# Optimization experiments

Hardware: AMD Instinct MI355X
Metric: run time of the kernel (lower is better)

The kernel has to match this reference:

```python
import jax, jax.numpy as jnp
import numpy as np

B, LQ, LK = 8, 1024, 1024
QD, KD, VD, OD, H = 512, 256, 256, 512, 8
HD = OD // H
SCALE = float(np.sqrt(HD))


def setup_inputs() -> dict:
    key = jax.random.key(0)
    ks = jax.random.split(key, 11)
    def lin(k, fan_in, fan_out):
        bound = 1.0 / np.sqrt(fan_in)
        kw, kb = jax.random.split(k)
        W = jax.random.uniform(kw, (fan_in, fan_out), jnp.float32, -bound, bound)
        b = jax.random.uniform(kb, (fan_out,), jnp.float32, -bound, bound)
        return W, b
    Wq, bq = lin(ks[0], QD, OD)
    Wk, bk = lin(ks[1], KD, OD)
    Wv, bv = lin(ks[2], VD, OD)
    Wo, bo = lin(ks[3], OD, OD)
    return {
        "query": jax.random.normal(ks[4], (B, LQ, QD), jnp.float32),
        "key": jax.random.normal(ks[5], (B, LK, KD), jnp.float32),
        "value": jax.random.normal(ks[6], (B, LK, VD), jnp.float32),
        "Wq": Wq, "bq": bq, "Wk": Wk, "bk": bk,
        "Wv": Wv, "bv": bv, "Wo": Wo, "bo": bo,
    }


def reference(query, key, value, Wq, bq, Wk, bk, Wv, bv, Wo, bo):
    b = query.shape[0]
    # project and split heads: (B, H, L, HD)
    q = (query @ Wq + bq).reshape(b, -1, H, HD).transpose(0, 2, 1, 3)
    k = (key @ Wk + bk).reshape(b, -1, H, HD).transpose(0, 2, 1, 3)
    v = (value @ Wv + bv).reshape(b, -1, H, HD).transpose(0, 2, 1, 3)
    scores = jnp.einsum("bhqd,bhkd->bhqk", q, k) / SCALE
    attention = jax.nn.softmax(scores, axis=-1)
    # dropout is identity in eval mode (reference uses eval semantics)
    out = jnp.einsum("bhqk,bhkd->bhqd", attention, v)
    out = out.transpose(0, 2, 1, 3).reshape(b, -1, H * HD)
    out = out @ Wo + bo
    return out, attention
```

## Files before the change

### kernel.cpp

```cpp
#include <hip/hip_runtime.h>

typedef __attribute__((ext_vector_type(8))) short s8b;
typedef __attribute__((ext_vector_type(4))) float f32x4;

#define MFMA_BF16(a, b, c) __builtin_amdgcn_mfma_f32_16x16x32_bf16((a), (b), (c), 0, 0, 0)

__device__ __forceinline__ short f2bf(float f) {
    unsigned u = __float_as_uint(f);
    u += 0x7fffu + ((u >> 16) & 1u);
    return (short)(u >> 16);
}

template <int OMODE, bool ABF16>
__global__ __launch_bounds__(256) void gemm_k(const void* __restrict__ Ain,
                                              const float* __restrict__ W,
                                              const float* __restrict__ bias,
                                              void* __restrict__ Cout,
                                              int K, float scale) {
    __shared__ short As[128][40];
    __shared__ short Bs[128][40];

    const int tid  = threadIdx.x;
    const int lane = tid & 63;
    const int wid  = tid >> 6;
    const int l15  = lane & 15, lhi = lane >> 4;
    const int wr   = wid >> 1, wc = wid & 1;
    const int bm   = blockIdx.x << 7;
    const int bn   = blockIdx.y << 7;

    const f32x4 zf = {0.f, 0.f, 0.f, 0.f};
    f32x4 acc[4][4];
#pragma unroll
    for (int i = 0; i < 4; ++i)
#pragma unroll
        for (int j = 0; j < 4; ++j) acc[i][j] = zf;

    const int arow = tid >> 1;
    const int ak0  = (tid & 1) << 4;
    const int bn_t = tid & 127;
    const int bk0  = (tid >> 7) << 4;

    const int nkt = K >> 5;
    for (int kt = 0; kt < nkt; ++kt) {
        __syncthreads();
        if (ABF16) {
            const short* src = (const short*)Ain + (size_t)(bm + arow) * K + (kt << 5) + ak0;
            *(s8b*)&As[arow][ak0]     = *(const s8b*)(src);
            *(s8b*)&As[arow][ak0 + 8] = *(const s8b*)(src + 8);
        } else {
            const float* src = (const float*)Ain + (size_t)(bm + arow) * K + (kt << 5) + ak0;
            s8b t0, t1;
#pragma unroll
            for (int i = 0; i < 8; ++i) { t0[i] = f2bf(src[i]); t1[i] = f2bf(src[i + 8]); }
            *(s8b*)&As[arow][ak0]     = t0;
            *(s8b*)&As[arow][ak0 + 8] = t1;
        }
        {
            s8b t0, t1;
#pragma unroll
            for (int j = 0; j < 8; ++j)
                t0[j] = f2bf(W[(size_t)((kt << 5) + bk0 + j) * 512 + bn + bn_t]);
#pragma unroll
            for (int j = 0; j < 8; ++j)
                t1[j] = f2bf(W[(size_t)((kt << 5) + bk0 + 8 + j) * 512 + bn + bn_t]);
            *(s8b*)&Bs[bn_t][bk0]     = t0;
            *(s8b*)&Bs[bn_t][bk0 + 8] = t1;
        }
        __syncthreads();
        s8b a[4], b[4];
#pragma unroll
        for (int rt = 0; rt < 4; ++rt)
            a[rt] = *(const s8b*)&As[(wr << 6) + (rt << 4) + l15][lhi << 3];
#pragma unroll
        for (int ct = 0; ct < 4; ++ct)
            b[ct] = *(const s8b*)&Bs[(wc << 6) + (ct << 4) + l15][lhi << 3];
#pragma unroll
        for (int rt = 0; rt < 4; ++rt)
#pragma unroll
            for (int ct = 0; ct < 4; ++ct)
                acc[rt][ct] = MFMA_BF16(a[rt], b[ct], acc[rt][ct]);
    }

#pragma unroll
    for (int rt = 0; rt < 4; ++rt)
#pragma unroll
        for (int ct = 0; ct < 4; ++ct) {
            const int col  = bn + (wc << 6) + (ct << 4) + l15;
            const float bv = bias[col];
#pragma unroll
            for (int r = 0; r < 4; ++r) {
                const int row = bm + (wr << 6) + (rt << 4) + (lhi << 2) + r;
                const float v = (acc[rt][ct][r] + bv) * scale;
                if (OMODE == 0) {
                    ((short*)Cout)[(size_t)row * 512 + col] = f2bf(v);
                } else if (OMODE == 1) {
                    const int bb = row >> 10, kv = row & 1023;
                    ((short*)Cout)[((size_t)(bb * 512 + col) << 10) + kv] = f2bf(v);
                } else {
                    ((float*)Cout)[(size_t)row * 512 + col] = v;
                }
            }
        }
}

__global__ __launch_bounds__(256) void attn_k(const short* __restrict__ Qp,
                                              const short* __restrict__ Kp,
                                              const short* __restrict__ Vt,
                                              float* __restrict__ attn,
                                              short* __restrict__ Oint) {
    __shared__ short Plds[4][32][72];

    const int tid = threadIdx.x;
    const int wid = tid >> 6, lane = tid & 63;
    const int l15 = lane & 15, lhi = lane >> 4;
    const int bid = blockIdx.x;
    const int qc = bid & 7, h = (bid >> 3) & 7, b = bid >> 6;
    const int q0 = (qc << 7) + (wid << 5);

    const size_t qbase = ((size_t)(b * 1024 + q0)) * 512 + h * 64;
    s8b aq[2][2];
#pragma unroll
    for (int rt = 0; rt < 2; ++rt)
#pragma unroll
        for (int ks = 0; ks < 2; ++ks)
            aq[rt][ks] = *(const s8b*)&Qp[qbase + (size_t)((rt << 4) + l15) * 512 + (ks << 5) + (lhi << 3)];

    float m8[8], l8[8];
#pragma unroll
    for (int i = 0; i < 8; ++i) { m8[i] = -1e30f; l8[i] = 0.f; }

    const size_t kbase = ((size_t)(b * 1024)) * 512 + h * 64;

    for (int kt = 0; kt < 16; ++kt) {
        s8b bk[4][2];
#pragma unroll
        for (int c = 0; c < 4; ++c)
#pragma unroll
            for (int ks = 0; ks < 2; ++ks)
                bk[c][ks] = *(const s8b*)&Kp[kbase + (size_t)((kt << 6) + (c << 4) + l15) * 512 + (ks << 5) + (lhi << 3)];
        const f32x4 zf = {0.f, 0.f, 0.f, 0.f};
        f32x4 s[2][4];
#pragma unroll
        for (int rt = 0; rt < 2; ++rt)
#pragma unroll
            for (int c = 0; c < 4; ++c) {
                s[rt][c] = zf;
                s[rt][c] = MFMA_BF16(aq[rt][0], bk[c][0], s[rt][c]);
                s[rt][c] = MFMA_BF16(aq[rt][1], bk[c][1], s[rt][c]);
            }
#pragma unroll
        for (int rt = 0; rt < 2; ++rt)
#pragma unroll
            for (int r = 0; r < 4; ++r) {
                const int idx = (rt << 2) + r;
                const float v0 = s[rt][0][r], v1 = s[rt][1][r];
                const float v2 = s[rt][2][r], v3 = s[rt][3][r];
                const float vm = fmaxf(fmaxf(v0, v1), fmaxf(v2, v3));
                const float mn = fmaxf(m8[idx], vm);
                const float corr = exp2f(m8[idx] - mn);
                const float add = exp2f(v0 - mn) + exp2f(v1 - mn) + exp2f(v2 - mn) + exp2f(v3 - mn);
                l8[idx] = l8[idx] * corr + add;
                m8[idx] = mn;
            }
    }
#pragma unroll
    for (int i = 0; i < 8; ++i) {
        float m = m8[i], l = l8[i];
#pragma unroll
        for (int mask = 1; mask <= 8; mask <<= 1) {
            const float mo = __shfl_xor(m, mask, 64);
            const float lo = __shfl_xor(l, mask, 64);
            const float mn = fmaxf(m, mo);
            l = l * exp2f(m - mn) + lo * exp2f(mo - mn);
            m = mn;
        }
        m8[i] = m;
        l8[i] = 1.0f / l;
    }

    const f32x4 zf = {0.f, 0.f, 0.f, 0.f};
    f32x4 o[2][4];
#pragma unroll
    for (int rt = 0; rt < 2; ++rt)
#pragma unroll
        for (int cd = 0; cd < 4; ++cd) o[rt][cd] = zf;

    const size_t vbase = ((size_t)(((b << 3) + h) << 6)) << 10;
    const size_t abase = ((size_t)(((b << 3) + h) * 1024 + q0)) << 10;

    for (int kt = 0; kt < 16; ++kt) {
        s8b bk[4][2];
#pragma unroll
        for (int c = 0; c < 4; ++c)
#pragma unroll
            for (int ks = 0; ks < 2; ++ks)
                bk[c][ks] = *(const s8b*)&Kp[kbase + (size_t)((kt << 6) + (c << 4) + l15) * 512 + (ks << 5) + (lhi << 3)];
        f32x4 s[2][4];
#pragma unroll
        for (int rt = 0; rt < 2; ++rt)
#pragma unroll
            for (int c = 0; c < 4; ++c) {
                s[rt][c] = zf;
                s[rt][c] = MFMA_BF16(aq[rt][0], bk[c][0], s[rt][c]);
                s[rt][c] = MFMA_BF16(aq[rt][1], bk[c][1], s[rt][c]);
            }
#pragma unroll
        for (int rt = 0; rt < 2; ++rt)
#pragma unroll
            for (int c = 0; c < 4; ++c)
#pragma unroll
                for (int r = 0; r < 4; ++r) {
                    const int idx = (rt << 2) + r;
                    s[rt][c][r] = exp2f(s[rt][c][r] - m8[idx]) * l8[idx];
                }
#pragma unroll
        for (int rt = 0; rt < 2; ++rt)
#pragma unroll
            for (int r = 0; r < 4; ++r) {
                const int prow = (rt << 4) + (lhi << 2) + r;
                const size_t ar = abase + ((size_t)prow << 10) + (kt << 6);
#pragma unroll
                for (int c = 0; c < 4; ++c) {
                    attn[ar + (c << 4) + l15] = s[rt][c][r];
                    Plds[wid][prow][(c << 4) + l15] = f2bf(s[rt][c][r]);
                }
            }
        s8b pa[2][2], bv[4][2];
#pragma unroll
        for (int rt = 0; rt < 2; ++rt)
#pragma unroll
            for (int ks = 0; ks < 2; ++ks)
                pa[rt][ks] = *(const s8b*)&Plds[wid][(rt << 4) + l15][(ks << 5) + (lhi << 3)];
#pragma unroll
        for (int cd = 0; cd < 4; ++cd)
#pragma unroll
            for (int ks = 0; ks < 2; ++ks)
                bv[cd][ks] = *(const s8b*)&Vt[vbase + (size_t)((cd << 4) + l15) * 1024 + (kt << 6) + (ks << 5) + (lhi << 3)];
#pragma unroll
        for (int rt = 0; rt < 2; ++rt)
#pragma unroll
            for (int cd = 0; cd < 4; ++cd) {
                o[rt][cd] = MFMA_BF16(pa[rt][0], bv[cd][0], o[rt][cd]);
                o[rt][cd] = MFMA_BF16(pa[rt][1], bv[cd][1], o[rt][cd]);
            }
    }

#pragma unroll
    for (int rt = 0; rt < 2; ++rt)
#pragma unroll
        for (int cd = 0; cd < 4; ++cd)
#pragma unroll
            for (int r = 0; r < 4; ++r) {
                const size_t orow =
                    ((size_t)(b * 1024 + q0 + (rt << 4) + (lhi << 2) + r)) * 512 + h * 64 + (cd << 4) + l15;
                Oint[orow] = f2bf(o[rt][cd][r]);
            }
}

extern "C" void kernel_launch(void* const* d_in, const int* in_sizes, int n_in,
                              void* d_out, int out_size, void* d_ws, size_t ws_size,
                              hipStream_t stream) {
    (void)in_sizes; (void)n_in; (void)out_size; (void)ws_size;

    const float* query = (const float*)d_in[0];
    const float* key   = (const float*)d_in[1];
    const float* value = (const float*)d_in[2];
    const float* Wq = (const float*)d_in[3];
    const float* bq = (const float*)d_in[4];
    const float* Wk = (const float*)d_in[5];
    const float* bk = (const float*)d_in[6];
    const float* Wv = (const float*)d_in[7];
    const float* bv = (const float*)d_in[8];
    const float* Wo = (const float*)d_in[9];
    const float* bo = (const float*)d_in[10];

    float* out  = (float*)d_out;
    float* attn = out + (size_t)8 * 1024 * 512;

    char* ws    = (char*)d_ws;
    short* Qp   = (short*)(ws);
    short* Kp   = (short*)(ws + (8u << 20));
    short* Vt   = (short*)(ws + (16u << 20));
    short* Oint = (short*)(ws + (24u << 20));

    const dim3 blk(256);
    const dim3 gg(64, 4);
    const float qscale = 0.18033688011112042f;

    gemm_k<0, false><<<gg, blk, 0, stream>>>(query, Wq, bq, Qp, 512, qscale);
    gemm_k<0, false><<<gg, blk, 0, stream>>>(key,   Wk, bk, Kp, 256, 1.0f);
    gemm_k<1, false><<<gg, blk, 0, stream>>>(value, Wv, bv, Vt, 256, 1.0f);
    attn_k<<<dim3(512), blk, 0, stream>>>(Qp, Kp, Vt, attn, Oint);
    gemm_k<2, true><<<gg, blk, 0, stream>>>(Oint, Wo, bo, out, 512, 1.0f);
}
```

Before: 463.1 us.

## Shrink GEMM tiles, add V transpose kernel, vectorize attention stores, remap blocks

The GEMM tile drops from 128x128 to 64x64 and the grid grows, giving more blocks to fill the CUs. The V projection now writes row-major output, and a separate LDS-based kernel transposes it, replacing the scattered strided stores. In the attention kernel, probabilities are staged in fp32 LDS so each wave can write the attention matrix with coalesced 16-byte stores instead of scalar ones. Block indices are also swizzled across batch and head. The cost is less operand reuse per GEMM tile, one extra kernel launch, and a larger workspace.

```diff
diff --git a/kernel.cpp b/kernel.cpp
--- a/kernel.cpp
+++ b/kernel.cpp
@@ -17,90 +17,108 @@
                                               const float* __restrict__ bias,
                                               void* __restrict__ Cout,
                                               int K, float scale) {
-    __shared__ short As[128][40];
-    __shared__ short Bs[128][40];
+    __shared__ short As[64][40];
+    __shared__ short Bs[64][40];
 
     const int tid  = threadIdx.x;
     const int lane = tid & 63;
     const int wid  = tid >> 6;
     const int l15  = lane & 15, lhi = lane >> 4;
     const int wr   = wid >> 1, wc = wid & 1;
-    const int bm   = blockIdx.x << 7;
-    const int bn   = blockIdx.y << 7;
+    const int bm   = blockIdx.x << 6;
+    const int bn   = blockIdx.y << 6;
 
     const f32x4 zf = {0.f, 0.f, 0.f, 0.f};
-    f32x4 acc[4][4];
-#pragma unroll
-    for (int i = 0; i < 4; ++i)
-#pragma unroll
-        for (int j = 0; j < 4; ++j) acc[i][j] = zf;
-
-    const int arow = tid >> 1;
-    const int ak0  = (tid & 1) << 4;
-    const int bn_t = tid & 127;
-    const int bk0  = (tid >> 7) << 4;
+    f32x4 acc[2][2];
+#pragma unroll
+    for (int i = 0; i < 2; ++i)
+#pragma unroll
+        for (int j = 0; j < 2; ++j) acc[i][j] = zf;
+
+    const int arow = tid >> 2;
+    const int ac8  = (tid & 3) << 3;
+    const int bn_t = tid & 63;
+    const int bk0  = (tid >> 6) << 3;
 
     const int nkt = K >> 5;
     for (int kt = 0; kt < nkt; ++kt) {
         __syncthreads();
         if (ABF16) {
-            const short* src = (const short*)Ain + (size_t)(bm + arow) * K + (kt << 5) + ak0;
-            *(s8b*)&As[arow][ak0]     = *(const s8b*)(src);
-            *(s8b*)&As[arow][ak0 + 8] = *(const s8b*)(src + 8);
+            const short* src = (const short*)Ain + (size_t)(bm + arow) * K + (kt << 5) + ac8;
+            *(s8b*)&As[arow][ac8] = *(const s8b*)(src);
         } else {
-            const float* src = (const float*)Ain + (size_t)(bm + arow) * K + (kt << 5) + ak0;
-            s8b t0, t1;
-#pragma unroll
-            for (int i = 0; i < 8; ++i) { t0[i] = f2bf(src[i]); t1[i] = f2bf(src[i + 8]); }
-            *(s8b*)&As[arow][ak0]     = t0;
-            *(s8b*)&As[arow][ak0 + 8] = t1;
+            const float* src = (const float*)Ain + (size_t)(bm + arow) * K + (kt << 5) + ac8;
+            s8b t;
+#pragma unroll
+            for (int i = 0; i < 8; ++i) t[i] = f2bf(src[i]);
+            *(s8b*)&As[arow][ac8] = t;
         }
         {
-            s8b t0, t1;
+            s8b t;
 #pragma unroll
             for (int j = 0; j < 8; ++j)
-                t0[j] = f2bf(W[(size_t)((kt << 5) + bk0 + j) * 512 + bn + bn_t]);
-#pragma unroll
-            for (int j = 0; j < 8; ++j)
-                t1[j] = f2bf(W[(size_t)((kt << 5) + bk0 + 8 + j) * 512 + bn + bn_t]);
-            *(s8b*)&Bs[bn_t][bk0]     = t0;
-            *(s8b*)&Bs[bn_t][bk0 + 8] = t1;
+                t[j] = f2bf(W[(size_t)((kt << 5) + bk0 + j) * 512 + bn + bn_t]);
+            *(s8b*)&Bs[bn_t][bk0] = t;
         }
         __syncthreads();
-        s8b a[4], b[4];
-#pragma unroll
-        for (int rt = 0; rt < 4; ++rt)
-            a[rt] = *(const s8b*)&As[(wr << 6) + (rt << 4) + l15][lhi << 3];
-#pragma unroll
-        for (int ct = 0; ct < 4; ++ct)
-            b[ct] = *(const s8b*)&Bs[(wc << 6) + (ct << 4) + l15][lhi << 3];
-#pragma unroll
-        for (int rt = 0; rt < 4; ++rt)
-#pragma unroll
-            for (int ct = 0; ct < 4; ++ct)
-                acc[rt][ct] = MFMA_BF16(a[rt], b[ct], acc[rt][ct]);
+        s8b a[2], bfr[2];
+#pragma unroll
+        for (int rt = 0; rt < 2; ++rt)
+            a[rt] = *(const s8b*)&As[(wr << 5) + (rt << 4) + l15][lhi << 3];
+#pragma unroll
+        for (int ct = 0; ct < 2; ++ct)
+            bfr[ct] = *(const s8b*)&Bs[(wc << 5) + (ct << 4) + l15][lhi << 3];
+#pragma unroll
+        for (int rt = 0; rt < 2; ++rt)
+#pragma unroll
+            for (int ct = 0; ct < 2; ++ct)
+                acc[rt][ct] = MFMA_BF16(a[rt], bfr[ct], acc[rt][ct]);
     }
 
 #pragma unroll
-    for (int rt = 0; rt < 4; ++rt)
-#pragma unroll
-        for (int ct = 0; ct < 4; ++ct) {
-            const int col  = bn + (wc << 6) + (ct << 4) + l15;
+    for (int rt = 0; rt < 2; ++rt)
+#pragma unroll
+        for (int ct = 0; ct < 2; ++ct) {
+            const int col  = bn + (wc << 5) + (ct << 4) + l15;
             const float bv = bias[col];
 #pragma unroll
             for (int r = 0; r < 4; ++r) {
-                const int row = bm + (wr << 6) + (rt << 4) + (lhi << 2) + r;
+                const int row = bm + (wr << 5) + (rt << 4) + (lhi << 2) + r;
                 const float v = (acc[rt][ct][r] + bv) * scale;
                 if (OMODE == 0) {
                     ((short*)Cout)[(size_t)row * 512 + col] = f2bf(v);
-                } else if (OMODE == 1) {
-                    const int bb = row >> 10, kv = row & 1023;
-                    ((short*)Cout)[((size_t)(bb * 512 + col) << 10) + kv] = f2bf(v);
                 } else {
                     ((float*)Cout)[(size_t)row * 512 + col] = v;
                 }
             }
         }
+}
+
+__global__ __launch_bounds__(256) void vtrans_k(const short* __restrict__ Vp,
+                                                short* __restrict__ Vt) {
+    __shared__ short Vs[64][72];
+
+    const int tid = threadIdx.x;
+    const int bid = blockIdx.x;
+    const int kvt = bid & 15, h = (bid >> 4) & 7, b = bid >> 7;
+    const int kv0 = kvt << 6;
+
+    const int r  = tid >> 2;
+    const int c0 = (tid & 3) << 4;
+    const short* src = Vp + (size_t)(b * 1024 + kv0 + r) * 512 + h * 64 + c0;
+    const s8b v0 = *(const s8b*)(src);
+    const s8b v1 = *(const s8b*)(src + 8);
+#pragma unroll
+    for (int i = 0; i < 8; ++i) Vs[c0 + i][r] = v0[i];
+#pragma unroll
+    for (int i = 0; i < 8; ++i) Vs[c0 + 8 + i][r] = v1[i];
+    __syncthreads();
+
+    const int d  = tid >> 2;
+    const int k0 = (tid & 3) << 4;
+    short* dst = Vt + ((size_t)(((b << 3) + h) << 6) + d) * 1024 + kv0 + k0;
+    *(s8b*)dst       = *(const s8b*)&Vs[d][k0];
+    *(s8b*)(dst + 8) = *(const s8b*)&Vs[d][k0 + 8];
 }
 
 __global__ __launch_bounds__(256) void attn_k(const short* __restrict__ Qp,
@@ -108,13 +126,14 @@
                                               const short* __restrict__ Vt,
                                               float* __restrict__ attn,
                                               short* __restrict__ Oint) {
-    __shared__ short Plds[4][32][72];
+    __shared__ float P32[4][32][68];
 
     const int tid = threadIdx.x;
     const int wid = tid >> 6, lane = tid & 63;
     const int l15 = lane & 15, lhi = lane >> 4;
     const int bid = blockIdx.x;
-    const int qc = bid & 7, h = (bid >> 3) & 7, b = bid >> 6;
+    const int w   = ((bid & 7) << 6) + (bid >> 3);
+    const int qc = w & 7, h = (w >> 3) & 7, b = w >> 6;
     const int q0 = (qc << 7) + (wid << 5);
 
     const size_t qbase = ((size_t)(b * 1024 + q0)) * 512 + h * 64;
@@ -130,6 +149,7 @@
     for (int i = 0; i < 8; ++i) { m8[i] = -1e30f; l8[i] = 0.f; }
 
     const size_t kbase = ((size_t)(b * 1024)) * 512 + h * 64;
+    const f32x4 zf = {0.f, 0.f, 0.f, 0.f};
 
     for (int kt = 0; kt < 16; ++kt) {
         s8b bk[4][2];
@@ -138,7 +158,6 @@
 #pragma unroll
             for (int ks = 0; ks < 2; ++ks)
                 bk[c][ks] = *(const s8b*)&Kp[kbase + (size_t)((kt << 6) + (c << 4) + l15) * 512 + (ks << 5) + (lhi << 3)];
-        const f32x4 zf = {0.f, 0.f, 0.f, 0.f};
         f32x4 s[2][4];
 #pragma unroll
         for (int rt = 0; rt < 2; ++rt)
@@ -178,7 +197,6 @@
         l8[i] = 1.0f / l;
     }
 
-    const f32x4 zf = {0.f, 0.f, 0.f, 0.f};
     f32x4 o[2][4];
 #pragma unroll
     for (int rt = 0; rt < 2; ++rt)
@@ -187,6 +205,9 @@
 
     const size_t vbase = ((size_t)(((b << 3) + h) << 6)) << 10;
     const size_t abase = ((size_t)(((b << 3) + h) * 1024 + q0)) << 10;
+
+    const int srow = lane >> 1;
+    const int scol = (lane & 1) << 5;
 
     for (int kt = 0; kt < 16; ++kt) {
         s8b bk[4][2];
@@ -211,26 +232,26 @@
 #pragma unroll
                 for (int r = 0; r < 4; ++r) {
                     const int idx = (rt << 2) + r;
-                    s[rt][c][r] = exp2f(s[rt][c][r] - m8[idx]) * l8[idx];
+                    const float p = exp2f(s[rt][c][r] - m8[idx]) * l8[idx];
+                    P32[wid][(rt << 4) + (lhi << 2) + r][(c << 4) + l15] = p;
                 }
-#pragma unroll
-        for (int rt = 0; rt < 2; ++rt)
-#pragma unroll
-            for (int r = 0; r < 4; ++r) {
-                const int prow = (rt << 4) + (lhi << 2) + r;
-                const size_t ar = abase + ((size_t)prow << 10) + (kt << 6);
-#pragma unroll
-                for (int c = 0; c < 4; ++c) {
-                    attn[ar + (c << 4) + l15] = s[rt][c][r];
-                    Plds[wid][prow][(c << 4) + l15] = f2bf(s[rt][c][r]);
-                }
-            }
-        s8b pa[2][2], bv[4][2];
-#pragma unroll
-        for (int rt = 0; rt < 2; ++rt)
-#pragma unroll
-            for (int ks = 0; ks < 2; ++ks)
-                pa[rt][ks] = *(const s8b*)&Plds[wid][(rt << 4) + l15][(ks << 5) + (lhi << 3)];
+        s8b pa[2][2];
+#pragma unroll
+        for (int rt = 0; rt < 2; ++rt)
+#pragma unroll
+            for (int ks = 0; ks < 2; ++ks) {
+                const float* pr = &P32[wid][(rt << 4) + l15][(ks << 5) + (lhi << 3)];
+                s8b t;
+#pragma unroll
+                for (int j = 0; j < 8; ++j) t[j] = f2bf(pr[j]);
+                pa[rt][ks] = t;
+            }
+#pragma unroll
+        for (int i = 0; i < 8; ++i) {
+            const f32x4 v = *(const f32x4*)&P32[wid][srow][scol + (i << 2)];
+            *(f32x4*)&attn[abase + ((size_t)srow << 10) + (kt << 6) + scol + (i << 2)] = v;
+        }
+        s8b bv[4][2];
 #pragma unroll
         for (int cd = 0; cd < 4; ++cd)
 #pragma unroll
@@ -280,16 +301,18 @@
     char* ws    = (char*)d_ws;
     short* Qp   = (short*)(ws);
     short* Kp   = (short*)(ws + (8u << 20));
-    short* Vt   = (short*)(ws + (16u << 20));
-    short* Oint = (short*)(ws + (24u << 20));
+    short* Vp   = (short*)(ws + (16u << 20));
+    short* Vt   = (short*)(ws + (24u << 20));
+    short* Oint = (short*)(ws + (32u << 20));
 
     const dim3 blk(256);
-    const dim3 gg(64, 4);
+    const dim3 gg(128, 8);
     const float qscale = 0.18033688011112042f;
 
     gemm_k<0, false><<<gg, blk, 0, stream>>>(query, Wq, bq, Qp, 512, qscale);
     gemm_k<0, false><<<gg, blk, 0, stream>>>(key,   Wk, bk, Kp, 256, 1.0f);
-    gemm_k<1, false><<<gg, blk, 0, stream>>>(value, Wv, bv, Vt, 256, 1.0f);
+    gemm_k<0, false><<<gg, blk, 0, stream>>>(value, Wv, bv, Vp, 256, 1.0f);
+    vtrans_k<<<dim3(1024), blk, 0, stream>>>(Vp, Vt);
     attn_k<<<dim3(512), blk, 0, stream>>>(Qp, Kp, Vt, attn, Oint);
     gemm_k<2, true><<<gg, blk, 0, stream>>>(Oint, Wo, bo, out, 512, 1.0f);
 }
```

Result: slower. 488.6 us (+5.5%).
